# Kernel tuning notes

Hardware: AMD Instinct MI355X
Metric: run time of the kernel (lower is better)

The kernel has to match this reference:

```python
import jax, jax.numpy as jnp
import numpy as np

MODES = 2
LC = 4
N = 6000
KNN = 10
NODES = 64
CH = MODES ** 2
M = N * 2 * (KNN + 1)  # total candidate couplings


def setup_inputs() -> dict:
    key = jax.random.key(0)
    ks = jax.random.split(key, 6)
    return {
        "CK_inputs": jax.random.normal(ks[0], (N, 2 * (KNN + 1), 3), dtype=jnp.float32),
        "W_in": jax.random.normal(ks[1], (3, NODES), dtype=jnp.float32) * 0.1,
        "b_in": jnp.zeros((NODES,), dtype=jnp.float32),
        "W_hid": jax.random.normal(ks[2], (LC - 1, NODES, NODES), dtype=jnp.float32) * 0.1,
        "b_hid": jnp.zeros((LC - 1, NODES), dtype=jnp.float32),
        "W_out": jax.random.normal(ks[3], (NODES, CH), dtype=jnp.float32) * 0.1,
        "b_out": jnp.zeros((CH,), dtype=jnp.float32),
        "coo": jax.random.randint(ks[4], (2, M), 0, N, dtype=jnp.int32),
    }


def _mlp(x, W_in, b_in, W_hid, b_hid, W_out, b_out):
    # MLP: 3 -> 64, (LC-1) hidden 64->64 layers, 64 -> CH; ReLU activations.
    h = jax.nn.relu(x @ W_in + b_in)
    for i in range(W_hid.shape[0]):  # small fixed layer count
        h = jax.nn.relu(h @ W_hid[i] + b_hid[i])
    return h @ W_out + b_out  # [M, CH]


def reference(CK_inputs, W_in, b_in, W_hid, b_hid, W_out, b_out, coo):
    C_stripped = _mlp(CK_inputs.reshape(-1, 3), W_in, b_in, W_hid, b_hid, W_out, b_out)  # [M, CH]
    D = MODES * N
    # Original: for channel ch = mi*MODES+mj, scatter C_stripped[:, ch] at indices coo*MODES+mj
    # (mj added to BOTH row and col, replicating the source exactly). Indices are
    # independent of mi, so sum over mi first, then one scatter-add per mj.
    vals = C_stripped.reshape(-1, MODES, MODES).sum(axis=1)  # [M, MODES]; axis1=mi, axis2=mj
    dense = jnp.zeros((D, D), dtype=CK_inputs.dtype)
    for mj in range(MODES):
        idx = coo * MODES + mj  # [2, M]
        dense = dense.at[idx[0], idx[1]].add(vals[:, mj])
    return dense
```

## Files before the change

### kernel.cpp

```cpp
#include <hip/hip_runtime.h>
#include <stdint.h>

#define NN    6000
#define KNNC  10
#define MM    (NN * 2 * (KNNC + 1))
#define DD    (2 * NN)
#define LCH   3
#define BLK   256

#define NV        ((long long)DD * DD / 4)
#define FILLGRID  2048
#define RB        256
#define RPL       4
#define MLPGRID   ((MM + RB - 1) / RB)
#define SCGRID    ((MM + BLK - 1) / BLK)

__global__ __launch_bounds__(BLK) void zero_fill(float* __restrict__ out) {
    const long long t0 = (long long)blockIdx.x * BLK + threadIdx.x;
    const long long stride = (long long)FILLGRID * BLK;
    float4 z = make_float4(0.f, 0.f, 0.f, 0.f);
    float4* outv = (float4*)out;
    for (long long i = t0; i < NV; i += stride) outv[i] = z;
}

__global__ __launch_bounds__(BLK, 2) void mlp(
    const float* __restrict__ CK,
    const float* __restrict__ Win,
    const float* __restrict__ bin,
    const float* __restrict__ Whid,
    const float* __restrict__ bhid,
    const float* __restrict__ Wout,
    const float* __restrict__ bout,
    float* __restrict__ vals)
{
    __shared__ float sW[64 * 64];
    __shared__ float sH[64 * RB];

    const int tid   = threadIdx.x;
    const int wave  = tid >> 6;
    const int lane  = tid & 63;
    const int jo    = wave << 4;
    const int rbase = blockIdx.x * RB;

    float x0[RPL], x1[RPL], x2[RPL];
#pragma unroll
    for (int r = 0; r < RPL; r++) {
        int m = rbase + r * 64 + lane;
        m = m < MM ? m : MM - 1;
        x0[r] = CK[m * 3 + 0];
        x1[r] = CK[m * 3 + 1];
        x2[r] = CK[m * 3 + 2];
    }

#pragma unroll
    for (int jj = 0; jj < 16; jj++) {
        const int j = jo + jj;
        const float w0 = Win[j], w1 = Win[64 + j], w2 = Win[128 + j];
        const float bj = bin[j];
#pragma unroll
        for (int r = 0; r < RPL; r++) {
            float a = fmaf(x2[r], w2, fmaf(x1[r], w1, fmaf(x0[r], w0, bj)));
            sH[j * RB + r * 64 + lane] = fmaxf(a, 0.f);
        }
    }
    __syncthreads();

#pragma unroll 1
    for (int l = 0; l < LCH; l++) {
        {
            const float4* __restrict__ Wg = (const float4*)(Whid + (l << 12));
            float4* __restrict__ sW4 = (float4*)sW;
#pragma unroll
            for (int i = 0; i < 4; i++) sW4[i * 256 + tid] = Wg[i * 256 + tid];
        }
        __syncthreads();

        float g[RPL][16];
#pragma unroll
        for (int jj = 0; jj < 16; jj++) {
            const float bj = bhid[(l << 6) + jo + jj];
#pragma unroll
            for (int r = 0; r < RPL; r++) g[r][jj] = bj;
        }

#pragma unroll 4
        for (int k = 0; k < 64; k++) {
            const float4 wa = *(const float4*)(sW + (k << 6) + jo);
            const float4 wb = *(const float4*)(sW + (k << 6) + jo + 4);
            const float4 wc = *(const float4*)(sW + (k << 6) + jo + 8);
            const float4 wd = *(const float4*)(sW + (k << 6) + jo + 12);
            float hk[RPL];
#pragma unroll
            for (int r = 0; r < RPL; r++) hk[r] = sH[k * RB + r * 64 + lane];
#pragma unroll
            for (int r = 0; r < RPL; r++) {
                g[r][0]  = fmaf(wa.x, hk[r], g[r][0]);
                g[r][1]  = fmaf(wa.y, hk[r], g[r][1]);
                g[r][2]  = fmaf(wa.z, hk[r], g[r][2]);
                g[r][3]  = fmaf(wa.w, hk[r], g[r][3]);
                g[r][4]  = fmaf(wb.x, hk[r], g[r][4]);
                g[r][5]  = fmaf(wb.y, hk[r], g[r][5]);
                g[r][6]  = fmaf(wb.z, hk[r], g[r][6]);
                g[r][7]  = fmaf(wb.w, hk[r], g[r][7]);
                g[r][8]  = fmaf(wc.x, hk[r], g[r][8]);
                g[r][9]  = fmaf(wc.y, hk[r], g[r][9]);
                g[r][10] = fmaf(wc.z, hk[r], g[r][10]);
                g[r][11] = fmaf(wc.w, hk[r], g[r][11]);
                g[r][12] = fmaf(wd.x, hk[r], g[r][12]);
                g[r][13] = fmaf(wd.y, hk[r], g[r][13]);
                g[r][14] = fmaf(wd.z, hk[r], g[r][14]);
                g[r][15] = fmaf(wd.w, hk[r], g[r][15]);
            }
        }
        __syncthreads();

#pragma unroll
        for (int jj = 0; jj < 16; jj++) {
#pragma unroll
            for (int r = 0; r < RPL; r++)
                sH[(jo + jj) * RB + r * 64 + lane] = fmaxf(g[r][jj], 0.f);
        }
        __syncthreads();
    }

    float v0[RPL], v1[RPL];
    const float b02 = bout[0] + bout[2], b13 = bout[1] + bout[3];
#pragma unroll
    for (int r = 0; r < RPL; r++) { v0[r] = b02; v1[r] = b13; }
#pragma unroll 8
    for (int k = 0; k < 64; k++) {
        const float4 wo = ((const float4*)Wout)[k];
        const float wxz = wo.x + wo.z, wyw = wo.y + wo.w;
#pragma unroll
        for (int r = 0; r < RPL; r++) {
            const float hk = sH[k * RB + r * 64 + lane];
            v0[r] = fmaf(hk, wxz, v0[r]);
            v1[r] = fmaf(hk, wyw, v1[r]);
        }
    }
#pragma unroll
    for (int r = 0; r < RPL; r++) {
        const int m = rbase + r * 64 + lane;
        if (m < MM) *(float2*)(vals + 2 * m) = make_float2(v0[r], v1[r]);
    }
}

__global__ __launch_bounds__(BLK) void scatter_add(
    const float* __restrict__ vals,
    const int* __restrict__ coo,
    float* __restrict__ out)
{
    const int t = blockIdx.x * BLK + threadIdx.x;
    if (t >= MM) return;
    const int r2 = coo[t] * 2;
    const int c2 = coo[MM + t] * 2;
    const float2 v = *(const float2*)(vals + 2 * t);
    const long long f0 = (long long)r2 * DD + c2;
    unsafeAtomicAdd(out + f0, v.x);
    unsafeAtomicAdd(out + f0 + DD + 1, v.y);
}

extern "C" void kernel_launch(void* const* d_in, const int* in_sizes, int n_in,
                              void* d_out, int out_size, void* d_ws, size_t ws_size,
                              hipStream_t stream) {
    const float* CK   = (const float*)d_in[0];
    const float* Win  = (const float*)d_in[1];
    const float* bin  = (const float*)d_in[2];
    const float* Whid = (const float*)d_in[3];
    const float* bhid = (const float*)d_in[4];
    const float* Wout = (const float*)d_in[5];
    const float* bout = (const float*)d_in[6];
    const int* coo    = (const int*)d_in[7];
    float* out        = (float*)d_out;
    float* vals       = (float*)d_ws;

    mlp<<<MLPGRID, BLK, 0, stream>>>(CK, Win, bin, Whid, bhid, Wout, bout, vals);
    zero_fill<<<FILLGRID, BLK, 0, stream>>>(out);
    scatter_add<<<SCGRID, BLK, 0, stream>>>(vals, coo, out);
}
```

Baseline: 699.3 us.

## Fuse scatter-add into MLP kernel, use memset, vectorize shared-memory row layout

The scatter-add is folded into the MLP kernel, so the intermediate vals buffer and one kernel launch go away. Each wave scatters one of the four rows each lane holds, with no redundant atomics. The custom zero-fill kernel is replaced by hipMemsetAsync. The MLP now keeps four consecutive rows per lane, which allows float4 input loads and float4 LDS reads and writes. The atomic scatter now runs inside the heavier MLP kernel, which may reduce how well the random atomics overlap with other work.

```diff
diff --git a/kernel.cpp b/kernel.cpp
--- a/kernel.cpp
+++ b/kernel.cpp
@@ -8,22 +8,12 @@
 #define LCH   3
 #define BLK   256
 
-#define NV        ((long long)DD * DD / 4)
-#define FILLGRID  2048
 #define RB        256
 #define RPL       4
 #define MLPGRID   ((MM + RB - 1) / RB)
-#define SCGRID    ((MM + BLK - 1) / BLK)
+#define OUTBYTES  ((size_t)DD * DD * 4)
 
-__global__ __launch_bounds__(BLK) void zero_fill(float* __restrict__ out) {
-    const long long t0 = (long long)blockIdx.x * BLK + threadIdx.x;
-    const long long stride = (long long)FILLGRID * BLK;
-    float4 z = make_float4(0.f, 0.f, 0.f, 0.f);
-    float4* outv = (float4*)out;
-    for (long long i = t0; i < NV; i += stride) outv[i] = z;
-}
-
-__global__ __launch_bounds__(BLK, 2) void mlp(
+__global__ __launch_bounds__(BLK, 2) void mlp_scatter(
     const float* __restrict__ CK,
     const float* __restrict__ Win,
     const float* __restrict__ bin,
@@ -31,7 +21,8 @@
     const float* __restrict__ bhid,
     const float* __restrict__ Wout,
     const float* __restrict__ bout,
-    float* __restrict__ vals)
+    const int* __restrict__ coo,
+    float* __restrict__ out)
 {
     __shared__ float sW[64 * 64];
     __shared__ float sH[64 * RB];
@@ -41,27 +32,27 @@
     const int lane  = tid & 63;
     const int jo    = wave << 4;
     const int rbase = blockIdx.x * RB;
+    const int mb0   = rbase + lane * 4;
+    const int mb    = mb0 < MM ? mb0 : MM - 4;
 
-    float x0[RPL], x1[RPL], x2[RPL];
-#pragma unroll
-    for (int r = 0; r < RPL; r++) {
-        int m = rbase + r * 64 + lane;
-        m = m < MM ? m : MM - 1;
-        x0[r] = CK[m * 3 + 0];
-        x1[r] = CK[m * 3 + 1];
-        x2[r] = CK[m * 3 + 2];
-    }
+    const float4 f0 = *(const float4*)(CK + mb * 3);
+    const float4 f1 = *(const float4*)(CK + mb * 3 + 4);
+    const float4 f2 = *(const float4*)(CK + mb * 3 + 8);
+    const float x0[RPL] = {f0.x, f0.w, f1.z, f2.y};
+    const float x1[RPL] = {f0.y, f1.x, f1.w, f2.z};
+    const float x2[RPL] = {f0.z, f1.y, f2.x, f2.w};
 
 #pragma unroll
     for (int jj = 0; jj < 16; jj++) {
         const int j = jo + jj;
         const float w0 = Win[j], w1 = Win[64 + j], w2 = Win[128 + j];
         const float bj = bin[j];
-#pragma unroll
-        for (int r = 0; r < RPL; r++) {
-            float a = fmaf(x2[r], w2, fmaf(x1[r], w1, fmaf(x0[r], w0, bj)));
-            sH[j * RB + r * 64 + lane] = fmaxf(a, 0.f);
-        }
+        float4 hv;
+        hv.x = fmaxf(fmaf(x2[0], w2, fmaf(x1[0], w1, fmaf(x0[0], w0, bj))), 0.f);
+        hv.y = fmaxf(fmaf(x2[1], w2, fmaf(x1[1], w1, fmaf(x0[1], w0, bj))), 0.f);
+        hv.z = fmaxf(fmaf(x2[2], w2, fmaf(x1[2], w1, fmaf(x0[2], w0, bj))), 0.f);
+        hv.w = fmaxf(fmaf(x2[3], w2, fmaf(x1[3], w1, fmaf(x0[3], w0, bj))), 0.f);
+        *(float4*)(sH + j * RB + lane * 4) = hv;
     }
     __syncthreads();
 
@@ -89,9 +80,8 @@
             const float4 wb = *(const float4*)(sW + (k << 6) + jo + 4);
             const float4 wc = *(const float4*)(sW + (k << 6) + jo + 8);
             const float4 wd = *(const float4*)(sW + (k << 6) + jo + 12);
-            float hk[RPL];
-#pragma unroll
-            for (int r = 0; r < RPL; r++) hk[r] = sH[k * RB + r * 64 + lane];
+            const float4 hv = *(const float4*)(sH + k * RB + lane * 4);
+            const float hk[RPL] = {hv.x, hv.y, hv.z, hv.w};
 #pragma unroll
             for (int r = 0; r < RPL; r++) {
                 g[r][0]  = fmaf(wa.x, hk[r], g[r][0]);
@@ -116,9 +106,12 @@
 
 #pragma unroll
         for (int jj = 0; jj < 16; jj++) {
-#pragma unroll
-            for (int r = 0; r < RPL; r++)
-                sH[(jo + jj) * RB + r * 64 + lane] = fmaxf(g[r][jj], 0.f);
+            float4 hv;
+            hv.x = fmaxf(g[0][jj], 0.f);
+            hv.y = fmaxf(g[1][jj], 0.f);
+            hv.z = fmaxf(g[2][jj], 0.f);
+            hv.w = fmaxf(g[3][jj], 0.f);
+            *(float4*)(sH + (jo + jj) * RB + lane * 4) = hv;
         }
         __syncthreads();
     }
@@ -131,33 +124,25 @@
     for (int k = 0; k < 64; k++) {
         const float4 wo = ((const float4*)Wout)[k];
         const float wxz = wo.x + wo.z, wyw = wo.y + wo.w;
-#pragma unroll
-        for (int r = 0; r < RPL; r++) {
-            const float hk = sH[k * RB + r * 64 + lane];
-            v0[r] = fmaf(hk, wxz, v0[r]);
-            v1[r] = fmaf(hk, wyw, v1[r]);
-        }
+        const float4 hv = *(const float4*)(sH + k * RB + lane * 4);
+        v0[0] = fmaf(hv.x, wxz, v0[0]);  v1[0] = fmaf(hv.x, wyw, v1[0]);
+        v0[1] = fmaf(hv.y, wxz, v0[1]);  v1[1] = fmaf(hv.y, wyw, v1[1]);
+        v0[2] = fmaf(hv.z, wxz, v0[2]);  v1[2] = fmaf(hv.z, wyw, v1[2]);
+        v0[3] = fmaf(hv.w, wxz, v0[3]);  v1[3] = fmaf(hv.w, wyw, v1[3]);
     }
-#pragma unroll
-    for (int r = 0; r < RPL; r++) {
-        const int m = rbase + r * 64 + lane;
-        if (m < MM) *(float2*)(vals + 2 * m) = make_float2(v0[r], v1[r]);
+
+    if (mb0 < MM) {
+        const int mrow = mb0 + wave;
+        const float sv0 = wave == 0 ? v0[0] : wave == 1 ? v0[1]
+                        : wave == 2 ? v0[2] : v0[3];
+        const float sv1 = wave == 0 ? v1[0] : wave == 1 ? v1[1]
+                        : wave == 2 ? v1[2] : v1[3];
+        const int r2 = coo[mrow] * 2;
+        const int c2 = coo[MM + mrow] * 2;
+        const long long f0i = (long long)r2 * DD + c2;
+        unsafeAtomicAdd(out + f0i, sv0);
+        unsafeAtomicAdd(out + f0i + DD + 1, sv1);
     }
-}
-
-__global__ __launch_bounds__(BLK) void scatter_add(
-    const float* __restrict__ vals,
-    const int* __restrict__ coo,
-    float* __restrict__ out)
-{
-    const int t = blockIdx.x * BLK + threadIdx.x;
-    if (t >= MM) return;
-    const int r2 = coo[t] * 2;
-    const int c2 = coo[MM + t] * 2;
-    const float2 v = *(const float2*)(vals + 2 * t);
-    const long long f0 = (long long)r2 * DD + c2;
-    unsafeAtomicAdd(out + f0, v.x);
-    unsafeAtomicAdd(out + f0 + DD + 1, v.y);
 }
 
 extern "C" void kernel_launch(void* const* d_in, const int* in_sizes, int n_in,
@@ -172,9 +157,8 @@
     const float* bout = (const float*)d_in[6];
     const int* coo    = (const int*)d_in[7];
     float* out        = (float*)d_out;
-    float* vals       = (float*)d_ws;
 
-    mlp<<<MLPGRID, BLK, 0, stream>>>(CK, Win, bin, Whid, bhid, Wout, bout, vals);
-    zero_fill<<<FILLGRID, BLK, 0, stream>>>(out);
-    scatter_add<<<SCGRID, BLK, 0, stream>>>(vals, coo, out);
+    hipMemsetAsync(out, 0, OUTBYTES, stream);
+    mlp_scatter<<<MLPGRID, BLK, 0, stream>>>(
+        CK, Win, bin, Whid, bhid, Wout, bout, coo, out);
 }
```

After: 662.4 us. 5.3% less time.
